# Kernel optimization log

Hardware: AMD Instinct MI355X
Metric: run time of the kernel (lower is better)

## Reference

```python
import jax, jax.numpy as jnp
import numpy as np

N_NODES = 50000
N_EDGES = 800000
IN_FEATURES = 256
HIDDEN = 128


def setup_inputs() -> dict:
    key = jax.random.key(0)
    k_x, k_r, k_c, k_v, k_w, k_b = jax.random.split(key, 6)
    x = jax.random.normal(k_x, (N_NODES, IN_FEATURES), dtype=jnp.float32)
    adj_row = jax.random.randint(k_r, (N_EDGES,), 0, N_NODES, dtype=jnp.int32)
    adj_col = jax.random.randint(k_c, (N_EDGES,), 0, N_NODES, dtype=jnp.int32)
    adj_val = jax.random.uniform(k_v, (N_EDGES,), dtype=jnp.float32)
    # Linear params: weight [hidden, in_features] (xavier-normal-ish), bias [hidden]
    std = float(np.sqrt(2.0 / (IN_FEATURES + HIDDEN)))
    W = jax.random.normal(k_w, (HIDDEN, IN_FEATURES), dtype=jnp.float32) * std
    b = jax.random.normal(k_b, (HIDDEN,), dtype=jnp.float32) * 0.01
    return {"x": x, "adj_row": adj_row, "adj_col": adj_col, "adj_val": adj_val, "W": W, "b": b}


def reference(x, adj_row, adj_col, adj_val, W, b):
    # support = Linear(x): [N, hidden]
    support = jnp.einsum('nf,hf->nh', x, W) + b
    # sparse adj @ support via edge-list gather + segment-sum scatter
    gathered = support[adj_col] * adj_val[:, None]          # [E, hidden]
    out = jax.ops.segment_sum(gathered, adj_row, num_segments=N_NODES)  # [N, hidden]
    return out
```

## Files before the change

### kernel.cpp

```cpp
#include <hip/hip_runtime.h>

#define N_NODES 50000
#define N_EDGES 800000
#define IN_F    256
#define HIDDEN  128

#define BUCKET_SZ 64
#define NB        782
#define NBP       1024
#define EBLOCK    2048
#define EBLOCKS   391
#define LBLOCKS   782
#define CAP       1344
#define OV_CAP    4096

typedef __attribute__((ext_vector_type(8))) short bf16x8;
typedef __attribute__((ext_vector_type(4))) float f32x4;

__device__ inline unsigned short f2bf(float f) {
    unsigned u = __float_as_uint(f);
    u += 0x7FFF + ((u >> 16) & 1);
    return (unsigned short)(u >> 16);
}
__device__ inline bf16x8 cvt8(float4 a, float4 b) {
    bf16x8 r;
    r[0] = (short)f2bf(a.x); r[1] = (short)f2bf(a.y);
    r[2] = (short)f2bf(a.z); r[3] = (short)f2bf(a.w);
    r[4] = (short)f2bf(b.x); r[5] = (short)f2bf(b.y);
    r[6] = (short)f2bf(b.z); r[7] = (short)f2bf(b.w);
    return r;
}
__device__ inline float bfLo(unsigned u) { return __uint_as_float(u << 16); }
__device__ inline float bfHi(unsigned u) { return __uint_as_float(u & 0xFFFF0000u); }

__global__ __launch_bounds__(256) void fused_linear_partition_kernel(
    const float* __restrict__ x, const float* __restrict__ W,
    const float* __restrict__ bias, unsigned short* __restrict__ support,
    const int* __restrict__ adj_row, const int* __restrict__ adj_col,
    const float* __restrict__ adj_val, int* __restrict__ cursor,
    int2* __restrict__ part, int4* __restrict__ ovbuf, int* __restrict__ ovcnt)
{
    __shared__ __align__(16) char smem[32768];
    const int tid = threadIdx.x;

    if (blockIdx.x < EBLOCKS) {
        int2* lbuf  = (int2*)smem;
        int*  lcnt  = (int*)(smem + 16384);
        int*  lcur  = (int*)(smem + 20480);
        int*  gbase = (int*)(smem + 24576);
        int*  tsum  = (int*)(smem + 28672);

        const int base = blockIdx.x * EBLOCK;
        const int n    = min(EBLOCK, N_EDGES - base);

        for (int i = tid; i < NBP; i += 256) lcnt[i] = 0;
        __syncthreads();

        unsigned pk[8]; float pv[8];
#pragma unroll
        for (int i = 0; i < 8; ++i) {
            int e = base + tid + i * 256;
            bool ok = e < N_EDGES;
            int ee = ok ? e : 0;
            int r = adj_row[ee], c = adj_col[ee];
            float v = adj_val[ee];
            if (ok) {
                unsigned bk = (unsigned)r >> 6;
                pk[i] = (bk << 22) | (((unsigned)r & 63u) << 16) | (unsigned)c;
                pv[i] = v;
                atomicAdd(&lcnt[bk], 1);
            } else pk[i] = 0xFFFFFFFFu;
        }
        __syncthreads();

        int s0 = lcnt[tid * 4], s1 = lcnt[tid * 4 + 1];
        int s2 = lcnt[tid * 4 + 2], s3 = lcnt[tid * 4 + 3];
        int mysum = s0 + s1 + s2 + s3;
        tsum[tid] = mysum;
        __syncthreads();
#pragma unroll
        for (int off = 1; off < 256; off <<= 1) {
            int t = (tid >= off) ? tsum[tid - off] : 0;
            __syncthreads();
            tsum[tid] += t;
            __syncthreads();
        }
        int ex = tsum[tid] - mysum;
        lcnt[tid * 4]     = ex;
        lcnt[tid * 4 + 1] = ex + s0;
        lcnt[tid * 4 + 2] = ex + s0 + s1;
        lcnt[tid * 4 + 3] = ex + s0 + s1 + s2;
        __syncthreads();

        for (int b = tid; b < NB; b += 256) {
            int c = lcnt[b + 1] - lcnt[b];
            gbase[b] = (c > 0) ? atomicAdd(&cursor[b], c) : 0;
            lcur[b]  = lcnt[b];
        }
        __syncthreads();

#pragma unroll
        for (int i = 0; i < 8; ++i) {
            if (pk[i] != 0xFFFFFFFFu) {
                unsigned bk = pk[i] >> 22;
                int p = atomicAdd(&lcur[bk], 1);
                lbuf[p] = make_int2((int)pk[i], __float_as_int(pv[i]));
            }
        }
        __syncthreads();

        for (int j = tid; j < n; j += 256) {
            int2 cv = lbuf[j];
            unsigned bk = ((unsigned)cv.x) >> 22;
            int loc = gbase[bk] + (j - lcnt[bk]);
            if (loc < CAP) {
                part[(size_t)bk * CAP + loc] = make_int2(cv.x & 0x3FFFFF, cv.y);
            } else {
                int op = atomicAdd(ovcnt, 1);
                if (op < OV_CAP) {
                    int r = (int)(bk * BUCKET_SZ) + ((cv.x >> 16) & 63);
                    ovbuf[op] = make_int4(r, cv.x & 0xFFFF, cv.y, 0);
                }
            }
        }
    } else {
        short* wfrag = (short*)smem;

        const int bid  = blockIdx.x - EBLOCKS;
        const int lane = tid & 63;
        const int wave = tid >> 6;
        const int quad = lane >> 4;
        const int l16  = lane & 15;

        int m = bid * 64 + wave * 16 + l16;
        if (m >= N_NODES) m = N_NODES - 1;
        const float* xrow = x + (size_t)m * IN_F;

        f32x4 acc[8];
#pragma unroll
        for (int s = 0; s < 8; ++s) acc[s] = (f32x4){0.f, 0.f, 0.f, 0.f};

        float4 a0 = *(const float4*)(xrow + quad * 8);
        float4 a1 = *(const float4*)(xrow + quad * 8 + 4);

#pragma unroll
        for (int half = 0; half < 2; ++half) {
#pragma unroll
            for (int it = 0; it < 8; ++it) {
                const int f   = it * 256 + tid;
                const int ln  = f & 63;
                const int s   = (f >> 6) & 7;
                const int kc  = f >> 9;
                const int row = s * 16 + (ln & 15);
                const int k0  = (half * 4 + kc) * 32 + (ln >> 4) * 8;
                const float* wp = W + (size_t)row * IN_F + k0;
                float4 b0 = *(const float4*)wp;
                float4 b1 = *(const float4*)(wp + 4);
                *(bf16x8*)(&wfrag[(size_t)f * 8]) = cvt8(b0, b1);
            }
            __syncthreads();

#pragma unroll
            for (int kc = 0; kc < 4; ++kc) {
                const int g = half * 4 + kc;
                bf16x8 af = cvt8(a0, a1);
                if (g < 7) {
                    const int k1 = (g + 1) * 32 + quad * 8;
                    a0 = *(const float4*)(xrow + k1);
                    a1 = *(const float4*)(xrow + k1 + 4);
                }
                const short* bbase = &wfrag[((size_t)(kc * 8) * 64 + lane) * 8];
#pragma unroll
                for (int s = 0; s < 8; ++s) {
                    bf16x8 bf = *(const bf16x8*)(bbase + (size_t)s * 64 * 8);
                    acc[s] = __builtin_amdgcn_mfma_f32_16x16x32_bf16(af, bf, acc[s], 0, 0, 0);
                }
            }
            __syncthreads();
        }

        const int rowBase = bid * 64 + wave * 16 + quad * 4;
#pragma unroll
        for (int reg = 0; reg < 4; ++reg) {
            const int r = rowBase + reg;
            if (r < N_NODES) {
#pragma unroll
                for (int s = 0; s < 8; ++s) {
                    const int col = s * 16 + l16;
                    float v = acc[s][reg] + bias[col];
                    support[(size_t)r * HIDDEN + col] = f2bf(v);
                }
            }
        }
    }
}

__global__ __launch_bounds__(512) void bucket_gather_kernel(
    const int* __restrict__ cursor, const int2* __restrict__ part,
    const unsigned int* __restrict__ support_u32, float* __restrict__ out)
{
    __shared__ int2 sbuf[CAP];
    __shared__ int  hist[BUCKET_SZ];
    __shared__ int  rp[BUCKET_SZ + 1];
    __shared__ int  cur[BUCKET_SZ];

    const int tid  = threadIdx.x;
    const int b    = blockIdx.x;
    const int n    = min(cursor[b], CAP);
    const int wave = tid >> 6;
    const int lane = tid & 63;

    if (tid < BUCKET_SZ) hist[tid] = 0;
    __syncthreads();

    int2 held[(CAP + 511) / 512];
    int  nheld = 0;
    const int2* pb = part + (size_t)b * CAP;
    for (int j = tid; j < n; j += 512) {
        int2 cv = pb[j];
        held[nheld++] = cv;
        atomicAdd(&hist[(cv.x >> 16) & 63], 1);
    }
    __syncthreads();

    if (tid < 64) {
        int v = hist[tid];
        int incl = v;
#pragma unroll
        for (int off = 1; off < 64; off <<= 1) {
            int t = __shfl_up(incl, off);
            if (tid >= off) incl += t;
        }
        rp[tid + 1] = incl;
        if (tid == 0) rp[0] = 0;
        cur[tid] = incl - v;
    }
    __syncthreads();

    for (int i = 0; i < nheld; ++i) {
        int r = (held[i].x >> 16) & 63;
        int p = atomicAdd(&cur[r], 1);
        sbuf[p] = held[i];
    }
    __syncthreads();

    const int rowLo = wave * 8;
#pragma unroll 1
    for (int r = rowLo; r < rowLo + 8; ++r) {
        const int grow = b * BUCKET_SZ + r;
        if (grow >= N_NODES) break;
        const int s = rp[r], e = rp[r + 1];
        float ax = 0.f, ay = 0.f;
        int j = s;
        for (; j + 3 < e; j += 4) {
            int2 c0 = sbuf[j],     c1 = sbuf[j + 1];
            int2 c2 = sbuf[j + 2], c3 = sbuf[j + 3];
            unsigned u0 = support_u32[(size_t)(c0.x & 0xFFFF) * 64 + lane];
            unsigned u1 = support_u32[(size_t)(c1.x & 0xFFFF) * 64 + lane];
            unsigned u2 = support_u32[(size_t)(c2.x & 0xFFFF) * 64 + lane];
            unsigned u3 = support_u32[(size_t)(c3.x & 0xFFFF) * 64 + lane];
            float v0 = __int_as_float(c0.y), v1 = __int_as_float(c1.y);
            float v2 = __int_as_float(c2.y), v3 = __int_as_float(c3.y);
            ax += v0 * bfLo(u0); ay += v0 * bfHi(u0);
            ax += v1 * bfLo(u1); ay += v1 * bfHi(u1);
            ax += v2 * bfLo(u2); ay += v2 * bfHi(u2);
            ax += v3 * bfLo(u3); ay += v3 * bfHi(u3);
        }
        for (; j < e; ++j) {
            int2 cv = sbuf[j];
            unsigned u = support_u32[(size_t)(cv.x & 0xFFFF) * 64 + lane];
            float v = __int_as_float(cv.y);
            ax += v * bfLo(u); ay += v * bfHi(u);
        }
        *(float2*)(out + (size_t)grow * HIDDEN + lane * 2) = make_float2(ax, ay);
    }
}

__global__ __launch_bounds__(256) void overflow_fix_kernel(
    const int* __restrict__ ovcnt, const int4* __restrict__ ovbuf,
    const unsigned int* __restrict__ support_u32, float* __restrict__ out)
{
    const int n    = min(*ovcnt, OV_CAP);
    const int wave = threadIdx.x >> 6;
    const int lane = threadIdx.x & 63;
    for (int j = wave; j < n; j += 4) {
        int4 o = ovbuf[j];
        unsigned u = support_u32[(size_t)o.y * 64 + lane];
        float v = __int_as_float(o.z);
        unsafeAtomicAdd(out + (size_t)o.x * HIDDEN + lane * 2,     v * bfLo(u));
        unsafeAtomicAdd(out + (size_t)o.x * HIDDEN + lane * 2 + 1, v * bfHi(u));
    }
}

extern "C" void kernel_launch(void* const* d_in, const int* in_sizes, int n_in,
                              void* d_out, int out_size, void* d_ws, size_t ws_size,
                              hipStream_t stream) {
    const float* x       = (const float*)d_in[0];
    const int*   adj_row = (const int*)d_in[1];
    const int*   adj_col = (const int*)d_in[2];
    const float* adj_val = (const float*)d_in[3];
    const float* W       = (const float*)d_in[4];
    const float* b       = (const float*)d_in[5];
    float* out = (float*)d_out;

    char* wsb = (char*)d_ws;
    const size_t off_support = 0;
    const size_t off_part    = off_support + (size_t)N_NODES * HIDDEN * 2;
    const size_t off_cursor  = off_part + (size_t)NB * CAP * 8;
    const size_t off_ovcnt   = off_cursor + (size_t)NB * 4;
    const size_t off_ovbuf   = (off_ovcnt + 4 + 15) & ~(size_t)15;

    unsigned short* support = (unsigned short*)(wsb + off_support);
    int2* part   = (int2*)(wsb + off_part);
    int*  cursor = (int*)(wsb + off_cursor);
    int*  ovcnt  = (int*)(wsb + off_ovcnt);
    int4* ovbuf  = (int4*)(wsb + off_ovbuf);

    hipMemsetAsync(cursor, 0, (size_t)(NB + 1) * 4, stream);

    fused_linear_partition_kernel<<<EBLOCKS + LBLOCKS, 256, 0, stream>>>(
        x, W, b, support, adj_row, adj_col, adj_val, cursor, part, ovbuf, ovcnt);
    bucket_gather_kernel<<<NB, 512, 0, stream>>>(
        cursor, part, (const unsigned int*)support, out);
    overflow_fix_kernel<<<1, 256, 0, stream>>>(
        ovcnt, ovbuf, (const unsigned int*)support, out);
}
```

Before: 187.2 us.

## Flatten per-wave row loop into a single software-pipelined 8-edge stream

Each wave now walks all edges of its 8 rows as one contiguous stream, issuing 8 independent support gathers per iteration and prefetching the next 8 LDS entries. Row boundaries are detected from the row field packed in each entry, and the accumulator is flushed whenever the row changes. Empty rows are zeroed in a separate pass. This removes the per-row loop and tail overhead and raises memory-level parallelism for short rows. The cost is more branching per edge, more registers for the prefetched entries, and sentinel padding in LDS.

```diff
diff --git a/kernel.cpp b/kernel.cpp
--- a/kernel.cpp
+++ b/kernel.cpp
@@ -13,6 +13,7 @@
 #define LBLOCKS   782
 #define CAP       1344
 #define OV_CAP    4096
+#define SENTINEL  (-65536)
 
 typedef __attribute__((ext_vector_type(8))) short bf16x8;
 typedef __attribute__((ext_vector_type(4))) float f32x4;
@@ -199,7 +200,7 @@
     const int* __restrict__ cursor, const int2* __restrict__ part,
     const unsigned int* __restrict__ support_u32, float* __restrict__ out)
 {
-    __shared__ int2 sbuf[CAP];
+    __shared__ int2 sbuf[CAP + 16];
     __shared__ int  hist[BUCKET_SZ];
     __shared__ int  rp[BUCKET_SZ + 1];
     __shared__ int  cur[BUCKET_SZ];
@@ -243,36 +244,69 @@
         sbuf[p] = held[i];
     }
     __syncthreads();
+    if (tid < 16) sbuf[n + tid] = make_int2(SENTINEL, 0);
+    __syncthreads();
 
     const int rowLo = wave * 8;
+    const int rowHi = rowLo + 8;
+    int jc   = rp[rowLo];
+    const int eIdx = rp[rowHi];
+
+    float ax = 0.f, ay = 0.f;
+    int curRow = -1;
+
+    int2 e0, e1, e2, e3, e4, e5, e6, e7;
+    if (jc < eIdx) {
+        e0 = sbuf[jc];     e1 = sbuf[jc + 1]; e2 = sbuf[jc + 2]; e3 = sbuf[jc + 3];
+        e4 = sbuf[jc + 4]; e5 = sbuf[jc + 5]; e6 = sbuf[jc + 6]; e7 = sbuf[jc + 7];
+    }
+
+    while (jc < eIdx) {
+        unsigned u0 = support_u32[(size_t)(e0.x & 0xFFFF) * 64 + lane];
+        unsigned u1 = support_u32[(size_t)(e1.x & 0xFFFF) * 64 + lane];
+        unsigned u2 = support_u32[(size_t)(e2.x & 0xFFFF) * 64 + lane];
+        unsigned u3 = support_u32[(size_t)(e3.x & 0xFFFF) * 64 + lane];
+        unsigned u4 = support_u32[(size_t)(e4.x & 0xFFFF) * 64 + lane];
+        unsigned u5 = support_u32[(size_t)(e5.x & 0xFFFF) * 64 + lane];
+        unsigned u6 = support_u32[(size_t)(e6.x & 0xFFFF) * 64 + lane];
+        unsigned u7 = support_u32[(size_t)(e7.x & 0xFFFF) * 64 + lane];
+
+        const int jn = jc + 8;
+        int2 f0, f1, f2, f3, f4, f5, f6, f7;
+        if (jn < eIdx) {
+            f0 = sbuf[jn];     f1 = sbuf[jn + 1]; f2 = sbuf[jn + 2]; f3 = sbuf[jn + 3];
+            f4 = sbuf[jn + 4]; f5 = sbuf[jn + 5]; f6 = sbuf[jn + 6]; f7 = sbuf[jn + 7];
+        }
+
+#define ACC_EDGE(K, EK, UK)                                                   \
+        if (jc + K < eIdx) {                                                  \
+            int r = EK.x >> 16;                                               \
+            if (r != curRow) {                                                \
+                if (curRow >= 0)                                              \
+                    *(float2*)(out + (size_t)(b * BUCKET_SZ + curRow) * HIDDEN\
+                               + lane * 2) = make_float2(ax, ay);             \
+                curRow = r; ax = 0.f; ay = 0.f;                               \
+            }                                                                 \
+            float v = __int_as_float(EK.y);                                   \
+            ax += v * bfLo(UK); ay += v * bfHi(UK);                           \
+        }
+        ACC_EDGE(0, e0, u0) ACC_EDGE(1, e1, u1) ACC_EDGE(2, e2, u2) ACC_EDGE(3, e3, u3)
+        ACC_EDGE(4, e4, u4) ACC_EDGE(5, e5, u5) ACC_EDGE(6, e6, u6) ACC_EDGE(7, e7, u7)
+#undef ACC_EDGE
+
+        e0 = f0; e1 = f1; e2 = f2; e3 = f3;
+        e4 = f4; e5 = f5; e6 = f6; e7 = f7;
+        jc = jn;
+    }
+    if (curRow >= 0)
+        *(float2*)(out + (size_t)(b * BUCKET_SZ + curRow) * HIDDEN + lane * 2)
+            = make_float2(ax, ay);
+
 #pragma unroll 1
-    for (int r = rowLo; r < rowLo + 8; ++r) {
+    for (int r = rowLo; r < rowHi; ++r) {
         const int grow = b * BUCKET_SZ + r;
-        if (grow >= N_NODES) break;
-        const int s = rp[r], e = rp[r + 1];
-        float ax = 0.f, ay = 0.f;
-        int j = s;
-        for (; j + 3 < e; j += 4) {
-            int2 c0 = sbuf[j],     c1 = sbuf[j + 1];
-            int2 c2 = sbuf[j + 2], c3 = sbuf[j + 3];
-            unsigned u0 = support_u32[(size_t)(c0.x & 0xFFFF) * 64 + lane];
-            unsigned u1 = support_u32[(size_t)(c1.x & 0xFFFF) * 64 + lane];
-            unsigned u2 = support_u32[(size_t)(c2.x & 0xFFFF) * 64 + lane];
-            unsigned u3 = support_u32[(size_t)(c3.x & 0xFFFF) * 64 + lane];
-            float v0 = __int_as_float(c0.y), v1 = __int_as_float(c1.y);
-            float v2 = __int_as_float(c2.y), v3 = __int_as_float(c3.y);
-            ax += v0 * bfLo(u0); ay += v0 * bfHi(u0);
-            ax += v1 * bfLo(u1); ay += v1 * bfHi(u1);
-            ax += v2 * bfLo(u2); ay += v2 * bfHi(u2);
-            ax += v3 * bfLo(u3); ay += v3 * bfHi(u3);
-        }
-        for (; j < e; ++j) {
-            int2 cv = sbuf[j];
-            unsigned u = support_u32[(size_t)(cv.x & 0xFFFF) * 64 + lane];
-            float v = __int_as_float(cv.y);
-            ax += v * bfLo(u); ay += v * bfHi(u);
-        }
-        *(float2*)(out + (size_t)grow * HIDDEN + lane * 2) = make_float2(ax, ay);
+        if (grow < N_NODES && rp[r] == rp[r + 1])
+            *(float2*)(out + (size_t)grow * HIDDEN + lane * 2) = make_float2(0.f, 0.f);
     }
 }
 
```

Measured after the change: 194.6 us. +4.0%, slower.
